# Optimization experiments

Hardware: AMD Instinct MI355X
Metric: run time of the kernel (lower is better)

## Reference

```python
import jax, jax.numpy as jnp
import numpy as np

N_WIRES = 5
N_OPS = 100000
BATCH = 64
TWO_PI = 6.283185307179586


def _apply_1q(state, U, axis):
    # Apply a shared 2x2 unitary U to the given wire axis of state [B,2,2,2,2,2].
    s = jnp.moveaxis(state, axis, -1)
    s = jnp.einsum('ij,...j->...i', U, s)
    return jnp.moveaxis(s, -1, axis)


def _apply_1q_batched(state, U, axis):
    # Per-batch 2x2 unitaries U: [B,2,2].
    s = jnp.moveaxis(state, axis, -1)
    s = jnp.einsum('bij,b...j->b...i', U, s)
    return jnp.moveaxis(s, -1, axis)


def _rot_unitaries(angles, types):
    # Build [n_ops,2,2] complex64 unitaries: type 0 -> RX, 1 -> RY, 2 -> RZ.
    half = angles * 0.5
    c = jnp.cos(half).astype(jnp.complex64)
    s = jnp.sin(half).astype(jnp.complex64)
    mis = (-1j) * s
    Urx = jnp.stack([jnp.stack([c, mis], -1), jnp.stack([mis, c], -1)], -2)
    Ury = jnp.stack([jnp.stack([c, -s], -1), jnp.stack([s, c], -1)], -2)
    e = jnp.exp((-1j) * half)  # complex64
    zero = jnp.zeros_like(e)
    Urz = jnp.stack([jnp.stack([e, zero], -1), jnp.stack([zero, jnp.conj(e)], -1)], -2)
    t = types[:, None, None]
    return jnp.where(t == 0, Urx, jnp.where(t == 1, Ury, Urz))


def _forward(x, gate_angles, gate_wires, gate_types):
    B = x.shape[0]
    # |00000> initial state per batch item
    state = jnp.zeros((B,) + (2,) * N_WIRES, jnp.complex64)
    state = state.at[(slice(None),) + (0,) * N_WIRES].set(1.0)

    # RxEncoder: RX(x[:, k]) on wire k
    half = x * 0.5
    c = jnp.cos(half).astype(jnp.complex64)
    s = jnp.sin(half).astype(jnp.complex64)
    for k in range(N_WIRES):
        U = jnp.stack([jnp.stack([c[:, k], (-1j) * s[:, k]], -1),
                       jnp.stack([(-1j) * s[:, k], c[:, k]], -1)], -2)  # [B,2,2]
        state = _apply_1q_batched(state, U, k + 1)

    # RandomLayer: long sequential chain of tiny gates on a resident state vector
    Us = _rot_unitaries(gate_angles, gate_types)
    branches = [lambda st, U, a=k + 1: _apply_1q(st, U, a) for k in range(N_WIRES)]

    def step(st, inp):
        U, w = inp
        return jax.lax.switch(w, branches, st, U), None

    state, _ = jax.lax.scan(step, state, (Us, gate_wires))

    # Measure: expval of PauliY on every wire -> [B, 5]
    Y = jnp.array([[0.0, -1j], [1j, 0.0]], jnp.complex64)
    outs = []
    for k in range(N_WIRES):
        ys = _apply_1q(state, Y, k + 1)
        outs.append(jnp.sum(jnp.conj(state) * ys, axis=tuple(range(1, N_WIRES + 1))).real)
    return jnp.stack(outs, -1)


def setup_inputs() -> dict:
    key = jax.random.key(0)
    k1, k2, k3, k4 = jax.random.split(key, 4)
    x = jax.random.normal(k1, (BATCH, N_WIRES), dtype=jnp.float32)
    gate_angles = jax.random.uniform(k2, (N_OPS,), dtype=jnp.float32) * TWO_PI
    gate_wires = jax.random.randint(k3, (N_OPS,), 0, N_WIRES, dtype=jnp.int32)
    gate_types = jax.random.randint(k4, (N_OPS,), 0, 3, dtype=jnp.int32)
    return {"x": x, "gate_angles": gate_angles, "gate_wires": gate_wires, "gate_types": gate_types}


def reference(x, gate_angles, gate_wires, gate_types):
    return _forward(x, gate_angles, gate_wires, gate_types)
```

## Files before the change

kernel.cpp:

```cpp
#include <hip/hip_runtime.h>


#define N_WIRES 5
#define BATCH 64
#define NBLK 128
#define NTHR 256
#define LANES (NBLK * NTHR)
#define CHUNK 4
#define QTUP (N_WIRES * 4)
#define NWAVE (NTHR / 64)

__device__ __forceinline__ void qmul(float* r, const float* b, const float* a) {
    r[0] = b[0]*a[0] - b[1]*a[1] - b[2]*a[2] - b[3]*a[3];
    r[1] = b[0]*a[1] + b[1]*a[0] + b[2]*a[3] - b[3]*a[2];
    r[2] = b[0]*a[2] - b[1]*a[3] + b[2]*a[0] + b[3]*a[1];
    r[3] = b[0]*a[3] + b[1]*a[2] - b[2]*a[1] + b[3]*a[0];
}

__device__ __forceinline__ void wave_reduce6(float* t) {
    for (int st = 1; st < 64; st <<= 1) {
        float o[QTUP];
        #pragma unroll
        for (int i = 0; i < QTUP; ++i) o[i] = __shfl_down(t[i], st, 64);
        #pragma unroll
        for (int w = 0; w < N_WIRES; ++w) {
            float r[4];
            qmul(r, &o[4*w], &t[4*w]);
            t[4*w+0] = r[0]; t[4*w+1] = r[1]; t[4*w+2] = r[2]; t[4*w+3] = r[3];
        }
    }
}

__global__ __launch_bounds__(NTHR)
void circuit_fused(const float* __restrict__ x,
                   const float* __restrict__ angles,
                   const int*   __restrict__ wires,
                   const int*   __restrict__ types,
                   int n_ops,
                   float* __restrict__ ws,
                   int*   __restrict__ ticket,
                   float* __restrict__ out)
{
    const int tid  = threadIdx.x;
    const int lane = blockIdx.x * NTHR + tid;

    float acc[N_WIRES][4];
    #pragma unroll
    for (int w = 0; w < N_WIRES; ++w) {
        acc[w][0] = 1.f; acc[w][1] = 0.f; acc[w][2] = 0.f; acc[w][3] = 0.f;
    }

    const int g0 = lane * CHUNK;
    if (g0 < n_ops) {
        float ang[CHUNK]; int wv[CHUNK], tv[CHUNK];
        float sv[CHUNK], cv[CHUNK];
        if (g0 + CHUNK <= n_ops) {
            const float4 a4 = *reinterpret_cast<const float4*>(angles + g0);
            const int4   w4 = *reinterpret_cast<const int4*>(wires + g0);
            const int4   t4 = *reinterpret_cast<const int4*>(types + g0);
            ang[0]=a4.x; ang[1]=a4.y; ang[2]=a4.z; ang[3]=a4.w;
            wv[0]=w4.x;  wv[1]=w4.y;  wv[2]=w4.z;  wv[3]=w4.w;
            tv[0]=t4.x;  tv[1]=t4.y;  tv[2]=t4.z;  tv[3]=t4.w;
            #pragma unroll
            for (int j = 0; j < CHUNK; ++j) __sincosf(0.5f*ang[j], &sv[j], &cv[j]);
        } else {
            #pragma unroll
            for (int j = 0; j < CHUNK; ++j) {
                const int g = g0 + j;
                const bool v = (g < n_ops);
                ang[j] = v ? angles[g] : 0.f;
                wv[j]  = v ? wires[g]  : 0;
                tv[j]  = v ? types[g]  : 0;
                __sincosf(0.5f*ang[j], &sv[j], &cv[j]);
                if (!v) { sv[j] = 0.f; cv[j] = 1.f; }
            }
        }
        #pragma unroll
        for (int j = 0; j < CHUNK; ++j) {
            const int w = wv[j], t = tv[j];
            const float s = sv[j], c = cv[j];
            float qw = acc[0][0], qx = acc[0][1], qy = acc[0][2], qz = acc[0][3];
            #pragma unroll
            for (int k = 1; k < N_WIRES; ++k) {
                const bool m = (w == k);
                qw = m ? acc[k][0] : qw;  qx = m ? acc[k][1] : qx;
                qy = m ? acc[k][2] : qy;  qz = m ? acc[k][3] : qz;
            }
            const float pw = (t == 0) ? -qx : (t == 1) ? -qy : -qz;
            const float px = (t == 0) ?  qw : (t == 1) ?  qz : -qy;
            const float py = (t == 0) ? -qz : (t == 1) ?  qw :  qx;
            const float pz = (t == 0) ?  qy : (t == 1) ? -qx :  qw;
            const float nw = c*qw + s*pw;
            const float nx = c*qx + s*px;
            const float ny = c*qy + s*py;
            const float nz = c*qz + s*pz;
            #pragma unroll
            for (int k = 0; k < N_WIRES; ++k) {
                const bool m = (w == k);
                acc[k][0] = m ? nw : acc[k][0];  acc[k][1] = m ? nx : acc[k][1];
                acc[k][2] = m ? ny : acc[k][2];  acc[k][3] = m ? nz : acc[k][3];
            }
        }
    }

    float t[QTUP];
    #pragma unroll
    for (int i = 0; i < QTUP; ++i) t[i] = acc[i >> 2][i & 3];
    wave_reduce6(t);

    __shared__ float lds[NWAVE][QTUP];
    __shared__ int   is_last;
    const int wave = tid >> 6;
    if ((tid & 63) == 0) {
        #pragma unroll
        for (int i = 0; i < QTUP; ++i) lds[wave][i] = t[i];
    }
    __syncthreads();
    if (tid == 0) {
        float r[QTUP];
        #pragma unroll
        for (int i = 0; i < QTUP; ++i) r[i] = lds[0][i];
        #pragma unroll
        for (int v = 1; v < NWAVE; ++v) {
            #pragma unroll
            for (int w = 0; w < N_WIRES; ++w) {
                float z[4];
                qmul(z, &lds[v][4*w], &r[4*w]);
                r[4*w+0]=z[0]; r[4*w+1]=z[1]; r[4*w+2]=z[2]; r[4*w+3]=z[3];
            }
        }
        #pragma unroll
        for (int i = 0; i < QTUP; ++i) ws[blockIdx.x * QTUP + i] = r[i];
        __threadfence();
        const int tk = atomicAdd(ticket, 1);
        is_last = (tk == NBLK - 1);
    }
    __syncthreads();
    if (!is_last) return;

    __threadfence();
    __shared__ float U[QTUP];
    float p[QTUP];
    if (tid < NBLK) {
        #pragma unroll
        for (int i = 0; i < QTUP; ++i) p[i] = ws[tid * QTUP + i];
        wave_reduce6(p);
        if ((tid & 63) == 0) {
            #pragma unroll
            for (int i = 0; i < QTUP; ++i) lds[tid >> 6][i] = p[i];
        }
    }
    __syncthreads();
    if (tid == 0) {
        #pragma unroll
        for (int w = 0; w < N_WIRES; ++w) {
            float z[4];
            qmul(z, &lds[1][4*w], &lds[0][4*w]);
            U[4*w+0]=z[0]; U[4*w+1]=z[1]; U[4*w+2]=z[2]; U[4*w+3]=z[3];
        }
    }
    __syncthreads();

    for (int o = tid; o < BATCH * N_WIRES; o += NTHR) {
        const int k = o % N_WIRES;
        const float xv = x[o];
        float sx, cx;
        __sincosf(0.5f * xv, &sx, &cx);
        const float* q = &U[4*k];
        const float v0r =  cx*q[0] - sx*q[1];
        const float v0i = -cx*q[3] + sx*q[2];
        const float v1r =  cx*q[2] + sx*q[3];
        const float v1i = -cx*q[1] - sx*q[0];
        out[o] = 2.f * (v0r * v1i - v0i * v1r);
    }
}

extern "C" void kernel_launch(void* const* d_in, const int* in_sizes, int n_in,
                              void* d_out, int out_size, void* d_ws, size_t ws_size,
                              hipStream_t stream) {
    const float* x      = (const float*)d_in[0];
    const float* angles = (const float*)d_in[1];
    const int*   wires  = (const int*)d_in[2];
    const int*   types  = (const int*)d_in[3];
    float* out = (float*)d_out;
    float* ws  = (float*)d_ws;
    int* ticket = (int*)((char*)d_ws + NBLK * QTUP * sizeof(float));

    const int n_ops = in_sizes[1];

    hipMemsetAsync(ticket, 0, sizeof(int), stream);
    circuit_fused<<<NBLK, NTHR, 0, stream>>>(x, angles, wires, types, n_ops,
                                             ws, ticket, out);
}
```

Before: 69.93 us.

## Split fused kernel into partials and finalize kernels, drop atomic ticket

The single fused kernel, which used a last-block atomic ticket plus a memset to finalize, becomes two kernel launches: one computes per-block quaternion partials, and a single 320-thread block reduces them and writes the outputs. This removes the memset launch, the thread fences and the atomic serialization. The cost is a second kernel launch and a dependency between kernels on the stream.

Result: faster. 66.55 us (-4.8%).

```diff
diff --git a/kernel.cpp b/kernel.cpp
--- a/kernel.cpp
+++ b/kernel.cpp
@@ -32,14 +32,11 @@
 }
 
 __global__ __launch_bounds__(NTHR)
-void circuit_fused(const float* __restrict__ x,
-                   const float* __restrict__ angles,
+void gate_partials(const float* __restrict__ angles,
                    const int*   __restrict__ wires,
                    const int*   __restrict__ types,
                    int n_ops,
-                   float* __restrict__ ws,
-                   int*   __restrict__ ticket,
-                   float* __restrict__ out)
+                   float* __restrict__ ws)
 {
     const int tid  = threadIdx.x;
     const int lane = blockIdx.x * NTHR + tid;
@@ -109,7 +106,6 @@
     wave_reduce6(t);
 
     __shared__ float lds[NWAVE][QTUP];
-    __shared__ int   is_last;
     const int wave = tid >> 6;
     if ((tid & 63) == 0) {
         #pragma unroll
@@ -131,17 +127,19 @@
         }
         #pragma unroll
         for (int i = 0; i < QTUP; ++i) ws[blockIdx.x * QTUP + i] = r[i];
-        __threadfence();
-        const int tk = atomicAdd(ticket, 1);
-        is_last = (tk == NBLK - 1);
     }
-    __syncthreads();
-    if (!is_last) return;
+}
 
-    __threadfence();
+__global__ __launch_bounds__(320)
+void finalize(const float* __restrict__ x,
+              const float* __restrict__ ws,
+              float* __restrict__ out)
+{
+    __shared__ float lds[2][QTUP];
     __shared__ float U[QTUP];
-    float p[QTUP];
+    const int tid = threadIdx.x;
     if (tid < NBLK) {
+        float p[QTUP];
         #pragma unroll
         for (int i = 0; i < QTUP; ++i) p[i] = ws[tid * QTUP + i];
         wave_reduce6(p);
@@ -161,9 +159,9 @@
     }
     __syncthreads();
 
-    for (int o = tid; o < BATCH * N_WIRES; o += NTHR) {
-        const int k = o % N_WIRES;
-        const float xv = x[o];
+    if (tid < BATCH * N_WIRES) {
+        const int k = tid % N_WIRES;
+        const float xv = x[tid];
         float sx, cx;
         __sincosf(0.5f * xv, &sx, &cx);
         const float* q = &U[4*k];
@@ -171,7 +169,7 @@
         const float v0i = -cx*q[3] + sx*q[2];
         const float v1r =  cx*q[2] + sx*q[3];
         const float v1i = -cx*q[1] - sx*q[0];
-        out[o] = 2.f * (v0r * v1i - v0i * v1r);
+        out[tid] = 2.f * (v0r * v1i - v0i * v1r);
     }
 }
 
@@ -184,11 +182,9 @@
     const int*   types  = (const int*)d_in[3];
     float* out = (float*)d_out;
     float* ws  = (float*)d_ws;
-    int* ticket = (int*)((char*)d_ws + NBLK * QTUP * sizeof(float));
 
     const int n_ops = in_sizes[1];
 
-    hipMemsetAsync(ticket, 0, sizeof(int), stream);
-    circuit_fused<<<NBLK, NTHR, 0, stream>>>(x, angles, wires, types, n_ops,
-                                             ws, ticket, out);
+    gate_partials<<<NBLK, NTHR, 0, stream>>>(angles, wires, types, n_ops, ws);
+    finalize<<<1, 320, 0, stream>>>(x, ws, out);
 }
```
